# Performance work log

Measured on AMD Instinct MI355X. Metric: run time of the kernel, lower is better.

The kernel has to match this reference:

```python
import jax, jax.numpy as jnp
import numpy as np

EMB = 384
HEAD_DIM = 64  # emb_size / num_head = 384 / 6
B, S = 8, 2048


def setup_inputs() -> dict:
    key = jax.random.key(0)
    k1, k2, k3, k4 = jax.random.split(key, 4)
    x = jax.random.normal(k1, (B, S, EMB), dtype=jnp.float32)
    # nn.Linear(emb, head_dim, bias=False): store as [in, out] so q = x @ W
    scale = 0.02
    Wq = jax.random.normal(k2, (EMB, HEAD_DIM), dtype=jnp.float32) * scale
    Wk = jax.random.normal(k3, (EMB, HEAD_DIM), dtype=jnp.float32) * scale
    Wv = jax.random.normal(k4, (EMB, HEAD_DIM), dtype=jnp.float32) * scale
    return {"x": x, "Wq": Wq, "Wk": Wk, "Wv": Wv}


def reference(x, Wq, Wk, Wv):
    # x: [B, S, C]
    q = jnp.einsum('bsc,cd->bsd', x, Wq)  # [B,S,D]
    k = jnp.einsum('bsc,cd->bsd', x, Wk)
    v = jnp.einsum('bsc,cd->bsd', x, Wv)
    scores = jnp.einsum('bid,bjd->bij', q, k) * (HEAD_DIM ** -0.5)  # [B,S,S]
    # causal mask: positions with tril==0 (j > i) set to -inf
    causal = jnp.tril(jnp.ones((S, S), dtype=bool))  # [S,S]
    scores = jnp.where(causal[None, :, :], scores, -jnp.inf)
    # NOTE: faithful to original — softmax over dim=1 (query axis), not -1.
    attn = jax.nn.softmax(scores, axis=1)  # [B,S,S]
    out = jnp.einsum('bij,bjd->bid', attn, v)  # [B,S,D]
    return out
```

## Files before the change

### kernel.cpp

```cpp
#include <hip/hip_runtime.h>
#include <hip/hip_bf16.h>
#include <math.h>

#define B_N 8
#define S_N 2048
#define C_N 384
#define D_N 64
#define NPART 4
#define NEG_BIG (-1e30f)

typedef __bf16 bf16x8 __attribute__((ext_vector_type(8)));
typedef float f32x4 __attribute__((ext_vector_type(4)));

static __device__ __forceinline__ bf16x8 ldfrag(const __bf16* p) {
  return *reinterpret_cast<const bf16x8*>(p);
}

static __device__ __forceinline__ void gload16(void* lds, const void* gsrc) {
  __builtin_amdgcn_global_load_lds(
      (const __attribute__((address_space(1))) unsigned int*)gsrc,
      (__attribute__((address_space(3))) unsigned int*)lds, 16, 0, 0);
}

__global__ __launch_bounds__(256) void w_prep(
    const float* __restrict__ Wq, const float* __restrict__ Wk,
    const float* __restrict__ Wv, __bf16* __restrict__ Wt) {
  const int idx = blockIdx.x * 256 + threadIdx.x;
  const int m = idx / (64 * C_N);
  const int r = idx % (64 * C_N);
  const int d = r / C_N;
  const int c = r % C_N;
  const float* W = (m == 0) ? Wq : (m == 1) ? Wk : Wv;
  Wt[idx] = (__bf16)W[c * 64 + d];
}

__global__ __launch_bounds__(384) void qkv_mfma(
    const float* __restrict__ x, const __bf16* __restrict__ Wt,
    __bf16* __restrict__ Q, __bf16* __restrict__ K, __bf16* __restrict__ Vt) {
  const int t = threadIdx.x;
  const int w = t >> 6, lane = t & 63, lr = lane & 15, lg = lane >> 4;
  const int mat = w >> 1, rh = w & 1;
  const int row0 = blockIdx.x * 32;
  const int ri = row0 + rh * 16 + lr;

  __shared__ __bf16 vtile[32][66];

  const float scl = (mat == 0) ? 0.125f : 1.0f;
  const float* xr = x + (size_t)ri * C_N;
  const __bf16* Wm = Wt + (size_t)mat * 64 * C_N;

  f32x4 acc[4];
#pragma unroll
  for (int nt = 0; nt < 4; ++nt) acc[nt] = {0.f, 0.f, 0.f, 0.f};

  float4 xa = *reinterpret_cast<const float4*>(xr + lg * 8);
  float4 xb = *reinterpret_cast<const float4*>(xr + lg * 8 + 4);
  bf16x8 bw[4];
#pragma unroll
  for (int nt = 0; nt < 4; ++nt)
    bw[nt] = ldfrag(Wm + (size_t)(nt * 16 + lr) * C_N + lg * 8);

  for (int kk = 0; kk < C_N / 32; ++kk) {
    const int kn = (kk + 1 < C_N / 32) ? kk + 1 : kk;
    const float4 xan = *reinterpret_cast<const float4*>(xr + kn * 32 + lg * 8);
    const float4 xbn = *reinterpret_cast<const float4*>(xr + kn * 32 + lg * 8 + 4);
    bf16x8 bwn[4];
#pragma unroll
    for (int nt = 0; nt < 4; ++nt)
      bwn[nt] = ldfrag(Wm + (size_t)(nt * 16 + lr) * C_N + kn * 32 + lg * 8);

    bf16x8 a;
    a[0] = (__bf16)(xa.x * scl); a[1] = (__bf16)(xa.y * scl);
    a[2] = (__bf16)(xa.z * scl); a[3] = (__bf16)(xa.w * scl);
    a[4] = (__bf16)(xb.x * scl); a[5] = (__bf16)(xb.y * scl);
    a[6] = (__bf16)(xb.z * scl); a[7] = (__bf16)(xb.w * scl);
#pragma unroll
    for (int nt = 0; nt < 4; ++nt)
      acc[nt] = __builtin_amdgcn_mfma_f32_16x16x32_bf16(a, bw[nt], acc[nt], 0, 0, 0);

    xa = xan; xb = xbn;
#pragma unroll
    for (int nt = 0; nt < 4; ++nt) bw[nt] = bwn[nt];
  }

  if (mat < 2) {
    __bf16* outp = (mat == 0) ? Q : K;
#pragma unroll
    for (int nt = 0; nt < 4; ++nt)
#pragma unroll
      for (int r = 0; r < 4; ++r)
        outp[(size_t)(row0 + rh * 16 + lg * 4 + r) * 64 + nt * 16 + lr] =
            (__bf16)acc[nt][r];
  } else {
#pragma unroll
    for (int nt = 0; nt < 4; ++nt)
#pragma unroll
      for (int r = 0; r < 4; ++r)
        vtile[rh * 16 + lg * 4 + r][nt * 16 + lr] = (__bf16)acc[nt][r];
  }
  __syncthreads();

  const int b = row0 >> 11, s0 = row0 & (S_N - 1);
  for (int idx = t; idx < 64 * 32; idx += 384) {
    const int d = idx >> 5, s2 = idx & 31;
    Vt[((size_t)b * D_N + d) * S_N + s0 + s2] = vtile[s2][d];
  }
}

__global__ __launch_bounds__(256) void col_stats(
    const __bf16* __restrict__ Q, const __bf16* __restrict__ K,
    float* __restrict__ zpart) {
  const int wg = blockIdx.x;
  const int b  = wg & 7;
  const int jb = (wg >> 3) & 31;
  const int h  = wg >> 8;
  const int j0 = jb * 64;

  const int t = threadIdx.x;
  const int q = t >> 6;
  const int lane = t & 63, lr = lane & 15, lg = lane >> 4;

  const int n = 32 - jb;
  const int itStart = jb + (n * h) / NPART;
  const int itEnd   = jb + (n * (h + 1)) / NPART;
  float* zout = zpart + (size_t)h * B_N * S_N + (size_t)b * S_N;

  if (itStart >= itEnd) {
    if (lg == 0) zout[j0 + q * 16 + lr] = 0.f;
    return;
  }

  __shared__ __align__(16) __bf16 QT[2][64][64];

  const __bf16* Qb = Q + (size_t)b * S_N * 64;
  const __bf16* Kb = K + (size_t)b * S_N * 64;

  const int krow = j0 + q * 16 + lr;
  const bf16x8 bk0 = ldfrag(Kb + (size_t)krow * 64 + lg * 8);
  const bf16x8 bk1 = ldfrag(Kb + (size_t)krow * 64 + 32 + lg * 8);

  const int r0 = t >> 3, c0 = t & 7;
  const int gq = c0 ^ (r0 & 7);

#define STAGE_Q(BUF, TILE) do { \
    gload16(&QT[BUF][r0][c0 * 8], Qb + (size_t)((TILE) * 64 + r0) * 64 + gq * 8); \
    gload16(&QT[BUF][r0 + 32][c0 * 8], \
            Qb + (size_t)((TILE) * 64 + r0 + 32) * 64 + gq * 8); \
  } while (0)

  STAGE_Q(0, itStart);
  __syncthreads();

  float z = 0.f;
  int cur = 0;
  for (int it = itStart; it < itEnd; ++it) {
    const int i0 = it * 64;
    if (it + 1 < itEnd) STAGE_Q(cur ^ 1, it + 1);

#pragma unroll
    for (int s = 0; s < 4; ++s) {
      const int arow = s * 16 + lr;
      const bf16x8 aq0 = ldfrag(&QT[cur][arow][(lg ^ (arow & 7)) * 8]);
      const bf16x8 aq1 = ldfrag(&QT[cur][arow][((4 + lg) ^ (arow & 7)) * 8]);
      f32x4 s4 = {0.f, 0.f, 0.f, 0.f};
      s4 = __builtin_amdgcn_mfma_f32_16x16x32_bf16(aq0, bk0, s4, 0, 0, 0);
      s4 = __builtin_amdgcn_mfma_f32_16x16x32_bf16(aq1, bk1, s4, 0, 0, 0);
      const int ibase = i0 + s * 16 + lg * 4;
      const int jg = j0 + q * 16 + lr;
      if (it == jb) {
#pragma unroll
        for (int r = 0; r < 4; ++r)
          if (ibase + r < jg) s4[r] = NEG_BIG;
      }
      float es = __expf(s4[0]) + __expf(s4[1]) + __expf(s4[2]) + __expf(s4[3]);
      es += __shfl_xor(es, 16);
      es += __shfl_xor(es, 32);
      z += es;
    }

    __syncthreads();
    cur ^= 1;
  }
#undef STAGE_Q

  if (lg == 0) zout[j0 + q * 16 + lr] = z;
}

__global__ __launch_bounds__(256) void attn_out(
    const __bf16* __restrict__ Q, const __bf16* __restrict__ K,
    const __bf16* __restrict__ Vt, const float* __restrict__ zpart,
    float* __restrict__ opart) {
  const int wg = blockIdx.x;
  const int b  = wg & 7;
  const int ib = (wg >> 3) & 31;
  const int h  = wg >> 8;

  const int t = threadIdx.x;
  const int s = t >> 6;
  const int lane = t & 63, lr = lane & 15, lg = lane >> 4;
  const int i0 = ib * 64;

  const int n = ib + 1;
  const int jbStart = (n * h) / NPART;
  const int jbEnd   = (n * (h + 1)) / NPART;

  float* op = opart + (size_t)h * B_N * S_N * D_N + (size_t)b * S_N * D_N;
  const int ibase = i0 + s * 16 + lg * 4;

  f32x4 o[4];
#pragma unroll
  for (int dt = 0; dt < 4; ++dt) o[dt] = {0.f, 0.f, 0.f, 0.f};

  if (jbStart < jbEnd) {
    __shared__ __align__(16) __bf16 KT[2][64][64];
    __shared__ __align__(16) __bf16 VT[2][64][64];
    __shared__ __align__(16) __bf16 P[4][16][72];

    const __bf16* Qb  = Q  + (size_t)b * S_N * 64;
    const __bf16* Kb  = K  + (size_t)b * S_N * 64;
    const __bf16* Vtb = Vt + (size_t)b * D_N * S_N;
    const float*  zp  = zpart + (size_t)b * S_N;

    const int r0 = t >> 3, c0 = t & 7;
    const int gq = c0 ^ (r0 & 7);

#define STAGE_KV(BUF, TJ0) do { \
      gload16(&KT[BUF][r0][c0 * 8], Kb + (size_t)((TJ0) + r0) * 64 + gq * 8); \
      gload16(&KT[BUF][r0 + 32][c0 * 8], \
              Kb + (size_t)((TJ0) + r0 + 32) * 64 + gq * 8); \
      gload16(&VT[BUF][r0][c0 * 8], Vtb + (size_t)r0 * S_N + (TJ0) + gq * 8); \
      gload16(&VT[BUF][r0 + 32][c0 * 8], \
              Vtb + (size_t)(r0 + 32) * S_N + (TJ0) + gq * 8); \
    } while (0)

    const int ri = i0 + s * 16 + lr;
    const bf16x8 aq0 = ldfrag(Qb + (size_t)ri * 64 + lg * 8);
    const bf16x8 aq1 = ldfrag(Qb + (size_t)ri * 64 + 32 + lg * 8);

    STAGE_KV(0, jbStart * 64);
    __syncthreads();

    int cur = 0;
    for (int jb = jbStart; jb < jbEnd; ++jb) {
      const int j0 = jb * 64;
      if (jb + 1 < jbEnd) STAGE_KV(cur ^ 1, j0 + 64);

#pragma unroll
      for (int jt = 0; jt < 4; ++jt) {
        const int krow = jt * 16 + lr;
        const bf16x8 bk0 = ldfrag(&KT[cur][krow][(lg ^ (krow & 7)) * 8]);
        const bf16x8 bk1 = ldfrag(&KT[cur][krow][((4 + lg) ^ (krow & 7)) * 8]);
        f32x4 s4 = {0.f, 0.f, 0.f, 0.f};
        s4 = __builtin_amdgcn_mfma_f32_16x16x32_bf16(aq0, bk0, s4, 0, 0, 0);
        s4 = __builtin_amdgcn_mfma_f32_16x16x32_bf16(aq1, bk1, s4, 0, 0, 0);
        const int jg = j0 + jt * 16 + lr;
        const float rz = 1.0f / (zp[jg] + zp[(size_t)B_N * S_N + jg] +
                                 zp[(size_t)2 * B_N * S_N + jg] +
                                 zp[(size_t)3 * B_N * S_N + jg]);
#pragma unroll
        for (int r = 0; r < 4; ++r) {
          const float pv = (jg <= ibase + r) ? __expf(s4[r]) * rz : 0.f;
          P[s][lg * 4 + r][jt * 16 + lr] = (__bf16)pv;
        }
      }

      const bf16x8 ap0 = ldfrag(&P[s][lr][lg * 8]);
      const bf16x8 ap1 = ldfrag(&P[s][lr][32 + lg * 8]);
#pragma unroll
      for (int dt = 0; dt < 4; ++dt) {
        const int vrow = dt * 16 + lr;
        const bf16x8 bv0 = ldfrag(&VT[cur][vrow][(lg ^ (vrow & 7)) * 8]);
        const bf16x8 bv1 = ldfrag(&VT[cur][vrow][((4 + lg) ^ (vrow & 7)) * 8]);
        o[dt] = __builtin_amdgcn_mfma_f32_16x16x32_bf16(ap0, bv0, o[dt], 0, 0, 0);
        o[dt] = __builtin_amdgcn_mfma_f32_16x16x32_bf16(ap1, bv1, o[dt], 0, 0, 0);
      }

      __syncthreads();
      cur ^= 1;
    }
#undef STAGE_KV
  }

#pragma unroll
  for (int dt = 0; dt < 4; ++dt)
#pragma unroll
    for (int r = 0; r < 4; ++r)
      op[(size_t)(ibase + r) * D_N + dt * 16 + lr] = o[dt][r];
}

__global__ __launch_bounds__(256) void combine(
    const float* __restrict__ opart, float* __restrict__ out) {
  const size_t idx = (size_t)blockIdx.x * 256 + threadIdx.x;
  const size_t stride = (size_t)B_N * S_N * D_N;
  out[idx] = opart[idx] + opart[stride + idx] + opart[2 * stride + idx] +
             opart[3 * stride + idx];
}

extern "C" void kernel_launch(void* const* d_in, const int* in_sizes, int n_in,
                              void* d_out, int out_size, void* d_ws, size_t ws_size,
                              hipStream_t stream) {
  (void)in_sizes; (void)n_in; (void)ws_size; (void)out_size;
  const float* x  = (const float*)d_in[0];
  const float* Wq = (const float*)d_in[1];
  const float* Wk = (const float*)d_in[2];
  const float* Wv = (const float*)d_in[3];
  float* out = (float*)d_out;

  __bf16* Qb = (__bf16*)d_ws;
  __bf16* Kb = Qb + (size_t)B_N * S_N * D_N;
  __bf16* Vt = Kb + (size_t)B_N * S_N * D_N;
  float* zpart = (float*)(Vt + (size_t)B_N * S_N * D_N);
  float* opart = zpart + (size_t)NPART * B_N * S_N;
  __bf16* Wt = (__bf16*)(opart + (size_t)NPART * B_N * S_N * D_N);

  w_prep<<<dim3(3 * 64 * C_N / 256), dim3(256), 0, stream>>>(Wq, Wk, Wv, Wt);
  qkv_mfma<<<dim3(B_N * S_N / 32), dim3(384), 0, stream>>>(x, Wt, Qb, Kb, Vt);
  col_stats<<<dim3(NPART * 32 * B_N), dim3(256), 0, stream>>>(Qb, Kb, zpart);
  attn_out<<<dim3(NPART * 32 * B_N), dim3(256), 0, stream>>>(Qb, Kb, Vt, zpart, opart);
  combine<<<dim3(B_N * S_N * D_N / 256), dim3(256), 0, stream>>>(opart, out);
}
```

Baseline: 74.24 us.

## Double attention tile height to 128 rows with 512-thread blocks

Both col_stats and attn_out now handle 128 rows per block with 8 waves instead of 64 rows with 4 waves, which halves the grid. The staged Q or K/V tiles are shared by twice as many waves, so less global traffic is needed per unit of work. The causal mask in col_stats becomes a per-element check on every iteration instead of only on the diagonal tile. In exchange the grid is smaller, causal load imbalance per block is coarser, and each block holds more registers.

```diff
diff --git a/kernel.cpp b/kernel.cpp
--- a/kernel.cpp
+++ b/kernel.cpp
@@ -107,22 +107,22 @@
   }
 }
 
-__global__ __launch_bounds__(256) void col_stats(
+__global__ __launch_bounds__(512) void col_stats(
     const __bf16* __restrict__ Q, const __bf16* __restrict__ K,
     float* __restrict__ zpart) {
   const int wg = blockIdx.x;
   const int b  = wg & 7;
-  const int jb = (wg >> 3) & 31;
-  const int h  = wg >> 8;
-  const int j0 = jb * 64;
+  const int jb = (wg >> 3) & 15;
+  const int h  = wg >> 7;
+  const int j0 = jb * 128;
 
   const int t = threadIdx.x;
   const int q = t >> 6;
   const int lane = t & 63, lr = lane & 15, lg = lane >> 4;
 
-  const int n = 32 - jb;
-  const int itStart = jb + (n * h) / NPART;
-  const int itEnd   = jb + (n * (h + 1)) / NPART;
+  const int n = 32 - 2 * jb;
+  const int itStart = 2 * jb + (n * h) / NPART;
+  const int itEnd   = 2 * jb + (n * (h + 1)) / NPART;
   float* zout = zpart + (size_t)h * B_N * S_N + (size_t)b * S_N;
 
   if (itStart >= itEnd) {
@@ -135,18 +135,15 @@
   const __bf16* Qb = Q + (size_t)b * S_N * 64;
   const __bf16* Kb = K + (size_t)b * S_N * 64;
 
-  const int krow = j0 + q * 16 + lr;
-  const bf16x8 bk0 = ldfrag(Kb + (size_t)krow * 64 + lg * 8);
-  const bf16x8 bk1 = ldfrag(Kb + (size_t)krow * 64 + 32 + lg * 8);
+  const int jg = j0 + q * 16 + lr;
+  const bf16x8 bk0 = ldfrag(Kb + (size_t)jg * 64 + lg * 8);
+  const bf16x8 bk1 = ldfrag(Kb + (size_t)jg * 64 + 32 + lg * 8);
 
   const int r0 = t >> 3, c0 = t & 7;
   const int gq = c0 ^ (r0 & 7);
 
-#define STAGE_Q(BUF, TILE) do { \
-    gload16(&QT[BUF][r0][c0 * 8], Qb + (size_t)((TILE) * 64 + r0) * 64 + gq * 8); \
-    gload16(&QT[BUF][r0 + 32][c0 * 8], \
-            Qb + (size_t)((TILE) * 64 + r0 + 32) * 64 + gq * 8); \
-  } while (0)
+#define STAGE_Q(BUF, TILE) \
+  gload16(&QT[BUF][r0][c0 * 8], Qb + (size_t)((TILE) * 64 + r0) * 64 + gq * 8)
 
   STAGE_Q(0, itStart);
   __syncthreads();
@@ -166,13 +163,10 @@
       s4 = __builtin_amdgcn_mfma_f32_16x16x32_bf16(aq0, bk0, s4, 0, 0, 0);
       s4 = __builtin_amdgcn_mfma_f32_16x16x32_bf16(aq1, bk1, s4, 0, 0, 0);
       const int ibase = i0 + s * 16 + lg * 4;
-      const int jg = j0 + q * 16 + lr;
-      if (it == jb) {
-#pragma unroll
-        for (int r = 0; r < 4; ++r)
-          if (ibase + r < jg) s4[r] = NEG_BIG;
-      }
-      float es = __expf(s4[0]) + __expf(s4[1]) + __expf(s4[2]) + __expf(s4[3]);
+      float es = 0.f;
+#pragma unroll
+      for (int r = 0; r < 4; ++r)
+        es += (ibase + r >= jg) ? __expf(s4[r]) : 0.f;
       es += __shfl_xor(es, 16);
       es += __shfl_xor(es, 32);
       z += es;
@@ -183,24 +177,24 @@
   }
 #undef STAGE_Q
 
-  if (lg == 0) zout[j0 + q * 16 + lr] = z;
-}
-
-__global__ __launch_bounds__(256) void attn_out(
+  if (lg == 0) zout[jg] = z;
+}
+
+__global__ __launch_bounds__(512) void attn_out(
     const __bf16* __restrict__ Q, const __bf16* __restrict__ K,
     const __bf16* __restrict__ Vt, const float* __restrict__ zpart,
     float* __restrict__ opart) {
   const int wg = blockIdx.x;
   const int b  = wg & 7;
-  const int ib = (wg >> 3) & 31;
-  const int h  = wg >> 8;
+  const int ib = (wg >> 3) & 15;
+  const int h  = wg >> 7;
 
   const int t = threadIdx.x;
   const int s = t >> 6;
   const int lane = t & 63, lr = lane & 15, lg = lane >> 4;
-  const int i0 = ib * 64;
-
-  const int n = ib + 1;
+  const int i0 = ib * 128;
+
+  const int n = 2 * ib + 2;
   const int jbStart = (n * h) / NPART;
   const int jbEnd   = (n * (h + 1)) / NPART;
 
@@ -214,7 +208,7 @@
   if (jbStart < jbEnd) {
     __shared__ __align__(16) __bf16 KT[2][64][64];
     __shared__ __align__(16) __bf16 VT[2][64][64];
-    __shared__ __align__(16) __bf16 P[4][16][72];
+    __shared__ __align__(16) __bf16 P[8][16][72];
 
     const __bf16* Qb  = Q  + (size_t)b * S_N * 64;
     const __bf16* Kb  = K  + (size_t)b * S_N * 64;
@@ -226,11 +220,7 @@
 
 #define STAGE_KV(BUF, TJ0) do { \
       gload16(&KT[BUF][r0][c0 * 8], Kb + (size_t)((TJ0) + r0) * 64 + gq * 8); \
-      gload16(&KT[BUF][r0 + 32][c0 * 8], \
-              Kb + (size_t)((TJ0) + r0 + 32) * 64 + gq * 8); \
       gload16(&VT[BUF][r0][c0 * 8], Vtb + (size_t)r0 * S_N + (TJ0) + gq * 8); \
-      gload16(&VT[BUF][r0 + 32][c0 * 8], \
-              Vtb + (size_t)(r0 + 32) * S_N + (TJ0) + gq * 8); \
     } while (0)
 
     const int ri = i0 + s * 16 + lr;
@@ -315,7 +305,7 @@
 
   w_prep<<<dim3(3 * 64 * C_N / 256), dim3(256), 0, stream>>>(Wq, Wk, Wv, Wt);
   qkv_mfma<<<dim3(B_N * S_N / 32), dim3(384), 0, stream>>>(x, Wt, Qb, Kb, Vt);
-  col_stats<<<dim3(NPART * 32 * B_N), dim3(256), 0, stream>>>(Qb, Kb, zpart);
-  attn_out<<<dim3(NPART * 32 * B_N), dim3(256), 0, stream>>>(Qb, Kb, Vt, zpart, opart);
+  col_stats<<<dim3(NPART * 16 * B_N), dim3(512), 0, stream>>>(Qb, Kb, zpart);
+  attn_out<<<dim3(NPART * 16 * B_N), dim3(512), 0, stream>>>(Qb, Kb, Vt, zpart, opart);
   combine<<<dim3(B_N * S_N * D_N / 256), dim3(256), 0, stream>>>(opart, out);
 }
```

Result: slower. 75.78 us (+2.1%).
